# Optimization experiments

Hardware: AMD Instinct MI355X
Metric: run time of the kernel (lower is better)

The kernel has to match this reference:

```python
import jax, jax.numpy as jnp
import numpy as np

N_NODES = 100000
N_EDGES = 1600000
DIMS = [128, 128, 128, 64]  # in, h1, h2, out


def setup_inputs() -> dict:
    key = jax.random.key(0)
    ks = jax.random.split(key, 12)
    inp = {
        "x": jax.random.normal(ks[0], (N_NODES, DIMS[0]), dtype=jnp.float32),
        "edge_index": jax.random.randint(ks[1], (2, N_EDGES), 0, N_NODES, dtype=jnp.int64),
        "edge_weights": jax.random.uniform(ks[2], (N_EDGES,), dtype=jnp.float32),
    }
    for i in range(3):
        inp[f"W{i+1}"] = jax.random.normal(ks[3 + 2 * i], (DIMS[i], DIMS[i + 1]), dtype=jnp.float32) * 0.05
        inp[f"b{i+1}"] = jax.random.normal(ks[4 + 2 * i], (DIMS[i + 1],), dtype=jnp.float32) * 0.01
    return inp


def gcn_conv(x, src, dst, w, W, b, n_nodes):
    # PyG GCNConv: linear transform, symmetric gcn_norm with self-loops (weight 1), scatter-add, bias.
    xw = x @ W                                            # [N, out]
    deg = jax.ops.segment_sum(w, dst, num_segments=n_nodes) + 1.0  # self-loop weight 1
    dinv = jnp.where(deg > 0, jax.lax.rsqrt(deg), 0.0)    # deg^{-1/2}
    norm = dinv[src] * w * dinv[dst]                      # [E]
    out = jax.ops.segment_sum(norm[:, None] * xw[src], dst, num_segments=n_nodes)
    out = out + (dinv * dinv)[:, None] * xw               # self-loop message
    return out + b


def reference(x, edge_index, edge_weights, W1, b1, W2, b2, W3, b3):
    src, dst = edge_index[0], edge_index[1]
    n = x.shape[0]
    # layer 1: GCNConv -> dropout(p=0) -> relu
    h = jax.nn.relu(gcn_conv(x, src, dst, edge_weights, W1, b1, n))
    # layer 2
    h = jax.nn.relu(gcn_conv(h, src, dst, edge_weights, W2, b2, n))
    # layer 3: activation 'none' -> Identity
    h = gcn_conv(h, src, dst, edge_weights, W3, b3, n)
    return h
```

## Files before the change

kernel.cpp:

```cpp
#include <hip/hip_runtime.h>
#include <hip/hip_fp16.h>
#include <math.h>


typedef __bf16 bf16x8 __attribute__((ext_vector_type(8)));
typedef float f32x4 __attribute__((ext_vector_type(4)));

union BF8 {
  unsigned short u[8];
  uint4 q;
  bf16x8 v;
};

union H8 {
  uint4 q;
  __half2 h2[4];
};

__device__ __forceinline__ unsigned short rne_bf16(float f) {
  unsigned u = __float_as_uint(f);
  u += 0x7fff + ((u >> 16) & 1);
  return (unsigned short)(u >> 16);
}
__device__ __forceinline__ float bf16_to_f(unsigned short h) {
  return __uint_as_float((unsigned)h << 16);
}

__device__ __forceinline__ void split_f32_to_bf(const float* av, BF8& ah, BF8& al) {
#pragma unroll
  for (int j = 0; j < 8; ++j) {
    unsigned short hb = rne_bf16(av[j]);
    ah.u[j] = hb;
    al.u[j] = rne_bf16(av[j] - bf16_to_f(hb));
  }
}

__device__ __forceinline__ void gemm_body_slice(const float* __restrict__ A,
    const float* __restrict__ W, int ldw, int col0,
    unsigned short* __restrict__ Ch, int ldc, int M, int bid) {
  constexpr int NF = 4;
  __shared__ __align__(16) unsigned short WT[2][64][128];
  const int t = threadIdx.x;
#pragma unroll
  for (int it = 0; it < 4; ++it) {
    int n = t & 63;
    int kc = it * 4 + (t >> 6);
    int k0 = kc * 8;
    BF8 hh, ll;
#pragma unroll
    for (int j = 0; j < 8; ++j) {
      float w = W[(size_t)(k0 + j) * ldw + col0 + n];
      unsigned short hb = rne_bf16(w);
      hh.u[j] = hb;
      ll.u[j] = rne_bf16(w - bf16_to_f(hb));
    }
    int kk = k0 ^ ((n & 7) << 3);
    *(uint4*)&WT[0][n][kk] = hh.q;
    *(uint4*)&WT[1][n][kk] = ll.q;
  }
  __syncthreads();

  const int wv = t >> 6;
  const int l = t & 63;
  const int lr = l & 15;
  const int lg = l >> 4;
  const int r0 = bid * 128 + wv * 32 + lr;
  const int r1 = r0 + 16;
  const bool v0 = r0 < M, v1 = r1 < M;
  const float* a0p = A + (size_t)r0 * 128;
  const float* a1p = A + (size_t)r1 * 128;

  f32x4 acc0[NF] = {}, acc1[NF] = {};
  float4 p00 = make_float4(0.f, 0.f, 0.f, 0.f), p01 = p00, p10 = p00, p11 = p00;
  if (v0) { p00 = *(const float4*)&a0p[lg * 8]; p01 = *(const float4*)&a0p[lg * 8 + 4]; }
  if (v1) { p10 = *(const float4*)&a1p[lg * 8]; p11 = *(const float4*)&a1p[lg * 8 + 4]; }
#pragma unroll 1
  for (int ks = 0; ks < 4; ++ks) {
    int nkb = ((ks < 3) ? (ks + 1) * 32 : ks * 32) + lg * 8;
    float4 q00 = make_float4(0.f, 0.f, 0.f, 0.f), q01 = q00, q10 = q00, q11 = q00;
    if (v0) { q00 = *(const float4*)&a0p[nkb]; q01 = *(const float4*)&a0p[nkb + 4]; }
    if (v1) { q10 = *(const float4*)&a1p[nkb]; q11 = *(const float4*)&a1p[nkb + 4]; }
    float av0[8] = {p00.x, p00.y, p00.z, p00.w, p01.x, p01.y, p01.z, p01.w};
    float av1[8] = {p10.x, p10.y, p10.z, p10.w, p11.x, p11.y, p11.z, p11.w};
    BF8 ah0, al0, ah1, al1;
    split_f32_to_bf(av0, ah0, al0);
    split_f32_to_bf(av1, ah1, al1);
    int kidx = ks * 32 + lg * 8;
#pragma unroll
    for (int nf = 0; nf < NF; ++nf) {
      int n = nf * 16 + lr;
      int kk = kidx ^ ((n & 7) << 3);
      BF8 bh, bl;
      bh.q = *(const uint4*)&WT[0][n][kk];
      bl.q = *(const uint4*)&WT[1][n][kk];
      acc0[nf] = __builtin_amdgcn_mfma_f32_16x16x32_bf16(ah0.v, bh.v, acc0[nf], 0, 0, 0);
      acc0[nf] = __builtin_amdgcn_mfma_f32_16x16x32_bf16(al0.v, bh.v, acc0[nf], 0, 0, 0);
      acc0[nf] = __builtin_amdgcn_mfma_f32_16x16x32_bf16(ah0.v, bl.v, acc0[nf], 0, 0, 0);
      acc1[nf] = __builtin_amdgcn_mfma_f32_16x16x32_bf16(ah1.v, bh.v, acc1[nf], 0, 0, 0);
      acc1[nf] = __builtin_amdgcn_mfma_f32_16x16x32_bf16(al1.v, bh.v, acc1[nf], 0, 0, 0);
      acc1[nf] = __builtin_amdgcn_mfma_f32_16x16x32_bf16(ah1.v, bl.v, acc1[nf], 0, 0, 0);
    }
    p00 = q00; p01 = q01; p10 = q10; p11 = q11;
  }
  const int ob = bid * 128 + wv * 32 + lg * 4;
#pragma unroll
  for (int j = 0; j < 4; ++j) {
    int orow = ob + j;
    if (orow < M) {
      unsigned short* hr = Ch + (size_t)orow * ldc + col0;
#pragma unroll
      for (int nf = 0; nf < NF; ++nf)
        hr[nf * 16 + lr] = __half_as_ushort(__float2half(acc0[nf][j]));
    }
    int orow1 = ob + 16 + j;
    if (orow1 < M) {
      unsigned short* hr = Ch + (size_t)orow1 * ldc + col0;
#pragma unroll
      for (int nf = 0; nf < NF; ++nf)
        hr[nf * 16 + lr] = __half_as_ushort(__float2half(acc1[nf][j]));
    }
  }
}

__global__ __launch_bounds__(256) void pre_gemm_fused_kernel(
    const float* __restrict__ x, const float* __restrict__ W1,
    unsigned short* __restrict__ Ch, int M,
    const int* __restrict__ ei, const float* __restrict__ ew,
    unsigned long long* __restrict__ packed, int* __restrict__ rank,
    int E, int edgeBlocks) {
  if ((int)blockIdx.x < edgeBlocks) {
    int e = blockIdx.x * 256 + threadIdx.x;
    if (e >= E) return;
    int d = ei[E + e];
    unsigned wfix = (unsigned)__float2uint_rn(ew[e] * 16777216.0f);
    unsigned long long inc = (1ULL << 32) | (unsigned long long)wfix;
    unsigned long long old = atomicAdd(&packed[d], inc);
    rank[e] = (int)(old >> 32);
  } else {
    int g = blockIdx.x - edgeBlocks;
    gemm_body_slice(x, W1, 128, (g & 1) * 64, Ch, 128, M, g >> 1);
  }
}

template <int NCOL>
__global__ __launch_bounds__(256) void gemm_mfma_kernel(
    const unsigned short* __restrict__ Ah, const float* __restrict__ W,
    unsigned short* __restrict__ Ch, int M) {
  constexpr int NF = NCOL / 16;
  __shared__ __align__(16) unsigned short WT[2][NCOL][128];
  const int t = threadIdx.x;
  constexpr int KC_PER_IT = 256 / NCOL;
#pragma unroll
  for (int it = 0; it < 16 / KC_PER_IT; ++it) {
    int n = t % NCOL;
    int kc = it * KC_PER_IT + t / NCOL;
    int k0 = kc * 8;
    BF8 hh, ll;
#pragma unroll
    for (int j = 0; j < 8; ++j) {
      float w = W[(size_t)(k0 + j) * NCOL + n];
      unsigned short hb = rne_bf16(w);
      hh.u[j] = hb;
      ll.u[j] = rne_bf16(w - bf16_to_f(hb));
    }
    int kk = k0 ^ ((n & 7) << 3);
    *(uint4*)&WT[0][n][kk] = hh.q;
    *(uint4*)&WT[1][n][kk] = ll.q;
  }
  __syncthreads();

  const int wv = t >> 6;
  const int l = t & 63;
  const int lr = l & 15;
  const int lg = l >> 4;
  const int r0 = blockIdx.x * 128 + wv * 32 + lr;
  const int r1 = r0 + 16;
  const bool v0 = r0 < M, v1 = r1 < M;
  const unsigned short* a0p = Ah + (size_t)r0 * 128;
  const unsigned short* a1p = Ah + (size_t)r1 * 128;

  f32x4 acc0[NF] = {}, acc1[NF] = {};
  uint4 ph0 = make_uint4(0, 0, 0, 0), ph1 = ph0;
  if (v0) ph0 = *(const uint4*)&a0p[lg * 8];
  if (v1) ph1 = *(const uint4*)&a1p[lg * 8];
#pragma unroll 1
  for (int ks = 0; ks < 4; ++ks) {
    int nkb = ((ks < 3) ? (ks + 1) * 32 : ks * 32) + lg * 8;
    uint4 qh0 = make_uint4(0, 0, 0, 0), qh1 = qh0;
    if (v0) qh0 = *(const uint4*)&a0p[nkb];
    if (v1) qh1 = *(const uint4*)&a1p[nkb];
    float av0[8], av1[8];
    {
      H8 uu; uu.q = ph0;
#pragma unroll
      for (int j = 0; j < 4; ++j) {
        float2 f = __half22float2(uu.h2[j]);
        av0[j * 2] = f.x; av0[j * 2 + 1] = f.y;
      }
      uu.q = ph1;
#pragma unroll
      for (int j = 0; j < 4; ++j) {
        float2 f = __half22float2(uu.h2[j]);
        av1[j * 2] = f.x; av1[j * 2 + 1] = f.y;
      }
    }
    BF8 ah0, al0, ah1, al1;
    split_f32_to_bf(av0, ah0, al0);
    split_f32_to_bf(av1, ah1, al1);
    int kidx = ks * 32 + lg * 8;
#pragma unroll
    for (int nf = 0; nf < NF; ++nf) {
      int n = nf * 16 + lr;
      int kk = kidx ^ ((n & 7) << 3);
      BF8 bh, bl;
      bh.q = *(const uint4*)&WT[0][n][kk];
      bl.q = *(const uint4*)&WT[1][n][kk];
      acc0[nf] = __builtin_amdgcn_mfma_f32_16x16x32_bf16(ah0.v, bh.v, acc0[nf], 0, 0, 0);
      acc0[nf] = __builtin_amdgcn_mfma_f32_16x16x32_bf16(al0.v, bh.v, acc0[nf], 0, 0, 0);
      acc0[nf] = __builtin_amdgcn_mfma_f32_16x16x32_bf16(ah0.v, bl.v, acc0[nf], 0, 0, 0);
      acc1[nf] = __builtin_amdgcn_mfma_f32_16x16x32_bf16(ah1.v, bh.v, acc1[nf], 0, 0, 0);
      acc1[nf] = __builtin_amdgcn_mfma_f32_16x16x32_bf16(al1.v, bh.v, acc1[nf], 0, 0, 0);
      acc1[nf] = __builtin_amdgcn_mfma_f32_16x16x32_bf16(ah1.v, bl.v, acc1[nf], 0, 0, 0);
    }
    ph0 = qh0; ph1 = qh1;
  }
  const int ob = blockIdx.x * 128 + wv * 32 + lg * 4;
#pragma unroll
  for (int j = 0; j < 4; ++j) {
    int orow = ob + j;
    if (orow < M) {
      unsigned short* hr = Ch + (size_t)orow * NCOL;
#pragma unroll
      for (int nf = 0; nf < NF; ++nf)
        hr[nf * 16 + lr] = __half_as_ushort(__float2half(acc0[nf][j]));
    }
    int orow1 = ob + 16 + j;
    if (orow1 < M) {
      unsigned short* hr = Ch + (size_t)orow1 * NCOL;
#pragma unroll
      for (int nf = 0; nf < NF; ++nf)
        hr[nf * 16 + lr] = __half_as_ushort(__float2half(acc1[nf][j]));
    }
  }
}

__global__ __launch_bounds__(1024) void scanA(const unsigned long long* __restrict__ packed,
    int* __restrict__ row_ptr, int* __restrict__ partials,
    float* __restrict__ dinv, int n) {
  __shared__ int sd[1024];
  int t = threadIdx.x;
  int i = blockIdx.x * 1024 + t;
  unsigned long long pv = (i < n) ? packed[i] : 0ULL;
  int v = (int)(pv >> 32);
  if (i < n) {
    float deg = 1.0f + (float)(unsigned)(pv & 0xffffffffULL) * (1.0f / 16777216.0f);
    dinv[i] = 1.0f / sqrtf(deg);
  }
  sd[t] = v;
  __syncthreads();
  for (int off = 1; off < 1024; off <<= 1) {
    int u = (t >= off) ? sd[t - off] : 0;
    __syncthreads();
    sd[t] += u;
    __syncthreads();
  }
  int incl = sd[t];
  if (i < n) row_ptr[i] = incl - v;
  if (t == 1023) partials[blockIdx.x] = incl;
}

__global__ __launch_bounds__(128) void scanB(int* partials, int nb) {
  __shared__ int sd[128];
  int t = threadIdx.x;
  int v = (t < nb) ? partials[t] : 0;
  sd[t] = v;
  __syncthreads();
  for (int off = 1; off < 128; off <<= 1) {
    int u = (t >= off) ? sd[t - off] : 0;
    __syncthreads();
    sd[t] += u;
    __syncthreads();
  }
  int incl = sd[t];
  partials[t] = incl - v;
  if (t == nb - 1) partials[255] = incl;
}

__global__ __launch_bounds__(1024) void scanC(int* row_ptr, const int* __restrict__ partials, int n) {
  int i = blockIdx.x * 1024 + threadIdx.x;
  if (i < n) row_ptr[i] += partials[blockIdx.x];
  if (i == 0) row_ptr[n] = partials[255];
}

__global__ __launch_bounds__(256) void fill_kernel(const int* __restrict__ ei,
    const float* __restrict__ ew, const float* __restrict__ dinv,
    const int* __restrict__ row_ptr, const int* __restrict__ rank,
    int2* __restrict__ epair, int E) {
  int e = blockIdx.x * 256 + threadIdx.x;
  if (e >= E) return;
  int s = ei[e], d = ei[E + e];
  float nw = dinv[s] * ew[e] * dinv[d];
  int p = row_ptr[d] + rank[e];
  epair[p] = make_int2(s, __float_as_int(nw));
}

template <int F, bool RELU, bool OUTF16>
__global__ __launch_bounds__(256) void agg_kernel(const unsigned short* __restrict__ xwh,
    const int* __restrict__ row_ptr, const int2* __restrict__ epair,
    const float* __restrict__ dinv, const float* __restrict__ bias,
    void* __restrict__ out, int Nn) {
  constexpr int LPN = F / 8;
  int t = blockIdx.x * 256 + threadIdx.x;
  int node = t / LPN;
  int lane = t % LPN;
  if (node >= Nn) return;
  const uint4* xh = (const uint4*)xwh;
  int start = row_ptr[node];
  int end = row_ptr[node + 1];
  float a0[8] = {}, a1[8] = {};
  int p = start;
  for (; p + 4 <= end; p += 4) {
    int2 e0 = epair[p];
    int2 e1 = epair[p + 1];
    int2 e2 = epair[p + 2];
    int2 e3 = epair[p + 3];
    H8 u0, u1, u2, u3;
    u0.q = xh[(size_t)e0.x * LPN + lane];
    u1.q = xh[(size_t)e1.x * LPN + lane];
    u2.q = xh[(size_t)e2.x * LPN + lane];
    u3.q = xh[(size_t)e3.x * LPN + lane];
    float n0 = __int_as_float(e0.y), n1 = __int_as_float(e1.y);
    float n2 = __int_as_float(e2.y), n3 = __int_as_float(e3.y);
#pragma unroll
    for (int j = 0; j < 4; ++j) {
      float2 f0 = __half22float2(u0.h2[j]);
      float2 f1 = __half22float2(u1.h2[j]);
      float2 f2 = __half22float2(u2.h2[j]);
      float2 f3 = __half22float2(u3.h2[j]);
      a0[j * 2]     = fmaf(n0, f0.x, a0[j * 2]);
      a0[j * 2 + 1] = fmaf(n0, f0.y, a0[j * 2 + 1]);
      a1[j * 2]     = fmaf(n1, f1.x, a1[j * 2]);
      a1[j * 2 + 1] = fmaf(n1, f1.y, a1[j * 2 + 1]);
      a0[j * 2]     = fmaf(n2, f2.x, a0[j * 2]);
      a0[j * 2 + 1] = fmaf(n2, f2.y, a0[j * 2 + 1]);
      a1[j * 2]     = fmaf(n3, f3.x, a1[j * 2]);
      a1[j * 2 + 1] = fmaf(n3, f3.y, a1[j * 2 + 1]);
    }
  }
  for (; p < end; ++p) {
    int2 pr = epair[p];
    float nw = __int_as_float(pr.y);
    H8 u; u.q = xh[(size_t)pr.x * LPN + lane];
#pragma unroll
    for (int j = 0; j < 4; ++j) {
      float2 f = __half22float2(u.h2[j]);
      a0[j * 2]     = fmaf(nw, f.x, a0[j * 2]);
      a0[j * 2 + 1] = fmaf(nw, f.y, a0[j * 2 + 1]);
    }
  }
  float di = dinv[node];
  float sw = di * di;
  H8 su; su.q = xh[(size_t)node * LPN + lane];
#pragma unroll
  for (int j = 0; j < 4; ++j) {
    float2 f = __half22float2(su.h2[j]);
    a0[j * 2]     = fmaf(sw, f.x, a0[j * 2]);
    a0[j * 2 + 1] = fmaf(sw, f.y, a0[j * 2 + 1]);
  }
  float4 b0 = ((const float4*)bias)[lane * 2];
  float4 b1 = ((const float4*)bias)[lane * 2 + 1];
  float o[8];
  o[0] = a0[0] + a1[0] + b0.x; o[1] = a0[1] + a1[1] + b0.y;
  o[2] = a0[2] + a1[2] + b0.z; o[3] = a0[3] + a1[3] + b0.w;
  o[4] = a0[4] + a1[4] + b1.x; o[5] = a0[5] + a1[5] + b1.y;
  o[6] = a0[6] + a1[6] + b1.z; o[7] = a0[7] + a1[7] + b1.w;
  if (RELU) {
#pragma unroll
    for (int j = 0; j < 8; ++j) o[j] = fmaxf(o[j], 0.f);
  }
  if constexpr (OUTF16) {
    H8 w;
#pragma unroll
    for (int j = 0; j < 4; ++j)
      w.h2[j] = __float22half2_rn(make_float2(o[j * 2], o[j * 2 + 1]));
    ((uint4*)out)[(size_t)node * LPN + lane] = w.q;
  } else {
    float4* of = (float4*)out + (size_t)node * LPN * 2 + lane * 2;
    of[0] = make_float4(o[0], o[1], o[2], o[3]);
    of[1] = make_float4(o[4], o[5], o[6], o[7]);
  }
}

extern "C" void kernel_launch(void* const* d_in, const int* in_sizes, int n_in,
                              void* d_out, int out_size, void* d_ws, size_t ws_size,
                              hipStream_t stream) {
  const float* x  = (const float*)d_in[0];
  const int*   ei = (const int*)d_in[1];
  const float* ew = (const float*)d_in[2];
  const float* W1 = (const float*)d_in[3];
  const float* b1 = (const float*)d_in[4];
  const float* W2 = (const float*)d_in[5];
  const float* b2 = (const float*)d_in[6];
  const float* W3 = (const float*)d_in[7];
  const float* b3 = (const float*)d_in[8];

  const int N = in_sizes[0] / 128;
  const int E = in_sizes[2];

  char* ws = (char*)d_ws;
  size_t off = 0;
  auto carve = [&](size_t bytes) -> void* {
    void* p = ws + off;
    off += (bytes + 255) & ~(size_t)255;
    return p;
  };
  unsigned long long* packed = (unsigned long long*)carve((size_t)N * 8);
  int*   rank    = (int*)carve((size_t)E * 4);
  float* dinv    = (float*)carve((size_t)N * 4);
  int*   row_ptr = (int*)carve((size_t)(N + 1) * 4);
  int*   parts   = (int*)carve(256 * 4);
  int2*  epair   = (int2*)carve((size_t)E * 8);
  unsigned short* bufH = (unsigned short*)carve((size_t)N * 128 * 2);
  unsigned short* bufI = (unsigned short*)carve((size_t)N * 128 * 2);
  (void)ws_size; (void)n_in; (void)out_size;

  const int nThreads = 256;
  int gE  = (E + nThreads - 1) / nThreads;
  int nb  = (N + 1023) / 1024;
  const int gMM = (N + 127) / 128;
  int gAgg128 = (N * 16 + nThreads - 1) / nThreads;
  int gAgg64  = (N * 8 + nThreads - 1) / nThreads;

  hipMemsetAsync(packed, 0, (size_t)N * 8, stream);
  pre_gemm_fused_kernel<<<gE + 2 * gMM, nThreads, 0, stream>>>(
      x, W1, bufH, N, ei, ew, packed, rank, E, gE);

  scanA<<<nb, 1024, 0, stream>>>(packed, row_ptr, parts, dinv, N);
  scanB<<<1, 128, 0, stream>>>(parts, nb);
  scanC<<<nb, 1024, 0, stream>>>(row_ptr, parts, N);
  fill_kernel<<<gE, nThreads, 0, stream>>>(ei, ew, dinv, row_ptr, rank, epair, E);

  agg_kernel<128, true, true><<<gAgg128, nThreads, 0, stream>>>(bufH, row_ptr, epair, dinv, b1, bufI, N);

  gemm_mfma_kernel<128><<<gMM, nThreads, 0, stream>>>(bufI, W2, bufH, N);
  agg_kernel<128, true, true><<<gAgg128, nThreads, 0, stream>>>(bufH, row_ptr, epair, dinv, b2, bufI, N);

  gemm_mfma_kernel<64><<<gMM, nThreads, 0, stream>>>(bufI, W3, bufH, N);
  agg_kernel<64, false, false><<<gAgg64, nThreads, 0, stream>>>(bufH, row_ptr, epair, dinv, b3, d_out, N);
}
```

Baseline: 335.0 us.

## Slice aggregation over feature columns so each block gathers a narrow column slab

Aggregation kernels now use a 2D grid: blockIdx.y selects a 16-feature slice, and each node gets 2 threads covering 32 bytes of the row instead of 16/8 threads covering the full row. All blocks for one slice gather the same narrow column slab of the feature matrix, which may raise L2/MALL hit rates for random neighbor gathers. The cost is that edge lists (row_ptr, epair) are re-read once per slice, and each gather now fetches short 32-byte segments.

```diff
diff --git a/kernel.cpp b/kernel.cpp
--- a/kernel.cpp
+++ b/kernel.cpp
@@ -305,16 +305,18 @@
 }
 
 template <int F, bool RELU, bool OUTF16>
-__global__ __launch_bounds__(256) void agg_kernel(const unsigned short* __restrict__ xwh,
+__global__ __launch_bounds__(256) void agg_sliced_kernel(
+    const unsigned short* __restrict__ xwh,
     const int* __restrict__ row_ptr, const int2* __restrict__ epair,
     const float* __restrict__ dinv, const float* __restrict__ bias,
     void* __restrict__ out, int Nn) {
-  constexpr int LPN = F / 8;
-  int t = blockIdx.x * 256 + threadIdx.x;
-  int node = t / LPN;
-  int lane = t % LPN;
+  constexpr int LPT = F / 8;
+  const int node = blockIdx.x * 128 + (threadIdx.x >> 1);
+  const int lane = threadIdx.x & 1;
+  const int sl = blockIdx.y;
   if (node >= Nn) return;
   const uint4* xh = (const uint4*)xwh;
+  const int co = sl * 2 + lane;
   int start = row_ptr[node];
   int end = row_ptr[node + 1];
   float a0[8] = {}, a1[8] = {};
@@ -325,10 +327,10 @@
     int2 e2 = epair[p + 2];
     int2 e3 = epair[p + 3];
     H8 u0, u1, u2, u3;
-    u0.q = xh[(size_t)e0.x * LPN + lane];
-    u1.q = xh[(size_t)e1.x * LPN + lane];
-    u2.q = xh[(size_t)e2.x * LPN + lane];
-    u3.q = xh[(size_t)e3.x * LPN + lane];
+    u0.q = xh[(size_t)e0.x * LPT + co];
+    u1.q = xh[(size_t)e1.x * LPT + co];
+    u2.q = xh[(size_t)e2.x * LPT + co];
+    u3.q = xh[(size_t)e3.x * LPT + co];
     float n0 = __int_as_float(e0.y), n1 = __int_as_float(e1.y);
     float n2 = __int_as_float(e2.y), n3 = __int_as_float(e3.y);
 #pragma unroll
@@ -350,7 +352,7 @@
   for (; p < end; ++p) {
     int2 pr = epair[p];
     float nw = __int_as_float(pr.y);
-    H8 u; u.q = xh[(size_t)pr.x * LPN + lane];
+    H8 u; u.q = xh[(size_t)pr.x * LPT + co];
 #pragma unroll
     for (int j = 0; j < 4; ++j) {
       float2 f = __half22float2(u.h2[j]);
@@ -360,15 +362,15 @@
   }
   float di = dinv[node];
   float sw = di * di;
-  H8 su; su.q = xh[(size_t)node * LPN + lane];
+  H8 su; su.q = xh[(size_t)node * LPT + co];
 #pragma unroll
   for (int j = 0; j < 4; ++j) {
     float2 f = __half22float2(su.h2[j]);
     a0[j * 2]     = fmaf(sw, f.x, a0[j * 2]);
     a0[j * 2 + 1] = fmaf(sw, f.y, a0[j * 2 + 1]);
   }
-  float4 b0 = ((const float4*)bias)[lane * 2];
-  float4 b1 = ((const float4*)bias)[lane * 2 + 1];
+  float4 b0 = ((const float4*)bias)[co * 2];
+  float4 b1 = ((const float4*)bias)[co * 2 + 1];
   float o[8];
   o[0] = a0[0] + a1[0] + b0.x; o[1] = a0[1] + a1[1] + b0.y;
   o[2] = a0[2] + a1[2] + b0.z; o[3] = a0[3] + a1[3] + b0.w;
@@ -383,9 +385,9 @@
 #pragma unroll
     for (int j = 0; j < 4; ++j)
       w.h2[j] = __float22half2_rn(make_float2(o[j * 2], o[j * 2 + 1]));
-    ((uint4*)out)[(size_t)node * LPN + lane] = w.q;
+    ((uint4*)out)[(size_t)node * LPT + co] = w.q;
   } else {
-    float4* of = (float4*)out + (size_t)node * LPN * 2 + lane * 2;
+    float4* of = (float4*)out + (size_t)node * (F / 4) + co * 2;
     of[0] = make_float4(o[0], o[1], o[2], o[3]);
     of[1] = make_float4(o[4], o[5], o[6], o[7]);
   }
@@ -428,8 +430,7 @@
   int gE  = (E + nThreads - 1) / nThreads;
   int nb  = (N + 1023) / 1024;
   const int gMM = (N + 127) / 128;
-  int gAgg128 = (N * 16 + nThreads - 1) / nThreads;
-  int gAgg64  = (N * 8 + nThreads - 1) / nThreads;
+  const int gAggX = (N + 127) / 128;
 
   hipMemsetAsync(packed, 0, (size_t)N * 8, stream);
   pre_gemm_fused_kernel<<<gE + 2 * gMM, nThreads, 0, stream>>>(
@@ -440,11 +441,14 @@
   scanC<<<nb, 1024, 0, stream>>>(row_ptr, parts, N);
   fill_kernel<<<gE, nThreads, 0, stream>>>(ei, ew, dinv, row_ptr, rank, epair, E);
 
-  agg_kernel<128, true, true><<<gAgg128, nThreads, 0, stream>>>(bufH, row_ptr, epair, dinv, b1, bufI, N);
+  agg_sliced_kernel<128, true, true><<<dim3(gAggX, 8), nThreads, 0, stream>>>(
+      bufH, row_ptr, epair, dinv, b1, bufI, N);
 
   gemm_mfma_kernel<128><<<gMM, nThreads, 0, stream>>>(bufI, W2, bufH, N);
-  agg_kernel<128, true, true><<<gAgg128, nThreads, 0, stream>>>(bufH, row_ptr, epair, dinv, b2, bufI, N);
+  agg_sliced_kernel<128, true, true><<<dim3(gAggX, 8), nThreads, 0, stream>>>(
+      bufH, row_ptr, epair, dinv, b2, bufI, N);
 
   gemm_mfma_kernel<64><<<gMM, nThreads, 0, stream>>>(bufI, W3, bufH, N);
-  agg_kernel<64, false, false><<<gAgg64, nThreads, 0, stream>>>(bufH, row_ptr, epair, dinv, b3, d_out, N);
-}
+  agg_sliced_kernel<64, false, false><<<dim3(gAggX, 4), nThreads, 0, stream>>>(
+      bufH, row_ptr, epair, dinv, b3, d_out, N);
+}
```

Result: slower. 816.6 us (+143.7%).
